# Performance work log

Hardware: AMD Instinct MI355X
Metric: run time of the kernel (lower is better)

## Reference

```python
import jax, jax.numpy as jnp
import numpy as np

RADIUS = 0.1      # ball-query radius; also max_dist in collision_error
THRESH = 0.001    # collision threshold
NSAMPLE = 4       # neighbors per query point
EPS = 1e-7
LOSS_WEIGHT = 1.0


def _face_normals(verts, faces):
    # verts: (b, n_v, 3), faces: (b, n_f, 3) int -> unit face normals (b, n_f, 3)
    tri = jax.vmap(lambda V, F: V[F])(verts, faces)  # (b, n_f, 3verts, 3xyz)
    e1 = tri[:, :, 1] - tri[:, :, 0]
    e2 = tri[:, :, 2] - tri[:, :, 0]
    fn = jnp.cross(e1, e2)
    return fn / (jnp.linalg.norm(fn, axis=-1, keepdims=True) + EPS)


def _vertex_normals(faces, fn, n_v):
    # sparse v2f bmm equivalent: average incident face normals per vertex
    def scatter(F, N):
        idx = F.reshape(-1)                    # (3*n_f,) face->vertex ids
        vals = jnp.repeat(N, 3, axis=0)        # each face normal to its 3 verts
        s = jnp.zeros((n_v, 3), N.dtype).at[idx].add(vals)
        c = jnp.zeros((n_v, 1), N.dtype).at[idx].add(jnp.float32(1.0))
        return s / (c + EPS)
    return jax.vmap(scatter)(faces, fn)        # (b, n_v, 3)


def _ball_query(new_xyz, xyz, radius, nsample):
    # PointNet++ ball query: first `nsample` points of xyz within radius of each
    # new_xyz point; unfilled slots repeat the first hit (0 if no hits).
    d2 = jnp.sum((new_xyz[:, :, None, :] - xyz[:, None, :, :]) ** 2, axis=-1)  # (b, nq, nv)
    within = d2 < radius * radius
    c = jnp.cumsum(within.astype(jnp.int32), axis=-1)
    n_within = c[..., -1]
    first_idx = jnp.argmax(within, axis=-1)    # 0 when no hits (matches CUDA kernel)
    slots = []
    for j in range(nsample):
        idx_j = jnp.argmax(within & (c == j + 1), axis=-1)
        slots.append(jnp.where(n_within > j, idx_j, first_idx))
    return jnp.stack(slots, axis=-1)           # (b, nq, nsample)


def _collision_loss(pred, h_state, h_faces):
    faces = jnp.swapaxes(h_faces, 1, 2)                 # (b, n_f, 3)
    human_verts = jnp.swapaxes(h_state, 1, 2)[..., :3]  # (b, n_v, 3)
    n_v = human_verts.shape[1]

    fn = _face_normals(human_verts, faces)
    vn = _vertex_normals(faces, fn, n_v)                # (b, n_v, 3)

    idx = _ball_query(pred, human_verts, RADIUS, NSAMPLE)      # (b, nq, K)
    gxyz = jax.vmap(lambda V, I: V[I])(human_verts, idx)       # (b, nq, K, 3)
    gn = jax.vmap(lambda V, I: V[I])(vn, idx)                  # (b, nq, K, 3)

    diff = pred[:, :, None, :] - gxyz
    gn = gn / (jnp.linalg.norm(gn, axis=-1, keepdims=True) + EPS)
    dot = jnp.sum(diff * gn, axis=-1)                   # (b, nq, K)
    valid_dot = (dot - THRESH) * (dot >= -RADIUS)       # max_dist = radius
    mask = valid_dot < 0
    per_pt = jnp.sum(valid_dot * mask / (jnp.sum(mask, axis=-1, keepdims=True) + EPS), axis=-1) ** 2
    avg_mask = per_pt > 0
    loss = jnp.sum(per_pt)                              # reduction='sum', weight=None
    loss = loss / (jnp.sum(avg_mask) + EPS)
    return LOSS_WEIGHT * loss


def setup_inputs() -> dict:
    key = jax.random.key(0)
    k1, k2, k3, k4 = jax.random.split(key, 4)
    bs, n_pred, n_v, n_f, C = 2, 8192, 6890, 13776, 6
    pred = jax.random.uniform(k1, (bs, n_pred, 3), dtype=jnp.float32)
    label = jax.random.uniform(k2, (bs, n_pred, 3), dtype=jnp.float32)
    h_state = jax.random.uniform(k3, (bs, C, n_v), dtype=jnp.float32)
    h_faces = jax.random.randint(k4, (bs, 3, n_f), 0, n_v, dtype=jnp.int32)
    return {"pred": pred, "label": label, "h_state": h_state, "h_faces": h_faces}


def reference(pred, label, h_state, h_faces):
    # label is unused by collision_error (kept for signature fidelity)
    return _collision_loss(pred, h_state, h_faces)
```

## Files before the change

### kernel.cpp

```cpp
#include <hip/hip_runtime.h>
#include <cstdint>
#include <climits>

#define EPSF 1e-7f
#define NCELL 1000
#define RPAD 0.10002f


__device__ __forceinline__ int cell_of(float x, float y, float z) {
    int cx = min(max((int)(x * 10.0f), 0), 9);
    int cy = min(max((int)(y * 10.0f), 0), 9);
    int cz = min(max((int)(z * 10.0f), 0), 9);
    return (cx * 10 + cy) * 10 + cz;
}

__global__ void k1_face_count(const float* __restrict__ hs,
                              const int* __restrict__ hf,
                              float* __restrict__ svec,
                              float* __restrict__ scnt,
                              int* __restrict__ counts,
                              int n_v, int n_f, int bs) {
    int t = blockIdx.x * blockDim.x + threadIdx.x;
    if (t < bs * n_f) {
        int b = t / n_f;
        int f = t - b * n_f;
        const int* fb = hf + (size_t)b * 3 * n_f;
        int i0 = fb[f];
        int i1 = fb[n_f + f];
        int i2 = fb[2 * n_f + f];
        const float* xs = hs + (size_t)b * 6 * n_v;
        const float* ys = xs + n_v;
        const float* zs = xs + 2 * n_v;
        float ax = xs[i0], ay = ys[i0], az = zs[i0];
        float bx = xs[i1], by = ys[i1], bz = zs[i1];
        float cx = xs[i2], cy = ys[i2], cz = zs[i2];
        float e1x = bx - ax, e1y = by - ay, e1z = bz - az;
        float e2x = cx - ax, e2y = cy - ay, e2z = cz - az;
        float fx = e1y * e2z - e1z * e2y;
        float fy = e1z * e2x - e1x * e2z;
        float fz = e1x * e2y - e1y * e2x;
        float nrm = sqrtf(fx * fx + fy * fy + fz * fz) + EPSF;
        fx /= nrm; fy /= nrm; fz /= nrm;
        float* sb = svec + (size_t)b * n_v * 3;
        float* cb = scnt + (size_t)b * n_v;
        atomicAdd(&sb[i0 * 3 + 0], fx);
        atomicAdd(&sb[i0 * 3 + 1], fy);
        atomicAdd(&sb[i0 * 3 + 2], fz);
        atomicAdd(&sb[i1 * 3 + 0], fx);
        atomicAdd(&sb[i1 * 3 + 1], fy);
        atomicAdd(&sb[i1 * 3 + 2], fz);
        atomicAdd(&sb[i2 * 3 + 0], fx);
        atomicAdd(&sb[i2 * 3 + 1], fy);
        atomicAdd(&sb[i2 * 3 + 2], fz);
        atomicAdd(&cb[i0], 1.0f);
        atomicAdd(&cb[i1], 1.0f);
        atomicAdd(&cb[i2], 1.0f);
    }
    if (t < bs * n_v) {
        int b = t / n_v;
        int v = t - b * n_v;
        const float* xs = hs + (size_t)b * 6 * n_v;
        float x = xs[v], y = xs[n_v + v], z = xs[2 * n_v + v];
        atomicAdd(&counts[b * NCELL + cell_of(x, y, z)], 1);
    }
}

__global__ void k2_build(const float* __restrict__ hs,
                         const float* __restrict__ svec,
                         const float* __restrict__ scnt,
                         const int* __restrict__ counts,
                         int* __restrict__ cellstart,
                         float4* __restrict__ vert,
                         float4* __restrict__ spk,
                         int n_v, int bs, int nvb) {
    __shared__ int cursor_l[NCELL];
    if (blockIdx.x < (unsigned)nvb) {
        int t = blockIdx.x * blockDim.x + threadIdx.x;
        if (t >= bs * n_v) return;
        int b = t / n_v;
        int v = t - b * n_v;
        float cc = scnt[t] + EPSF;
        float vx = svec[t * 3 + 0] / cc;
        float vy = svec[t * 3 + 1] / cc;
        float vz = svec[t * 3 + 2] / cc;
        float nrm = sqrtf(vx * vx + vy * vy + vz * vz) + EPSF;
        const float* xs = hs + (size_t)b * 6 * n_v;
        float x = xs[v], y = xs[n_v + v], z = xs[2 * n_v + v];
        vert[2 * (size_t)t + 0] = make_float4(x, y, z, 0.0f);
        vert[2 * (size_t)t + 1] = make_float4(vx / nrm, vy / nrm, vz / nrm, 0.0f);
        return;
    }
    int batch = blockIdx.x - nvb;
    if (threadIdx.x < 64) {
        int lane = threadIdx.x;
        int local[16];
        int mysum = 0;
        #pragma unroll
        for (int k = 0; k < 16; ++k) {
            int c = lane * 16 + k;
            int v = (c < NCELL) ? counts[batch * NCELL + c] : 0;
            local[k] = v;
            mysum += v;
        }
        int s = mysum;
        #pragma unroll
        for (int off = 1; off < 64; off <<= 1) {
            int n = __shfl_up(s, off);
            if (lane >= off) s += n;
        }
        int excl = s - mysum;
        #pragma unroll
        for (int k = 0; k < 16; ++k) {
            int c = lane * 16 + k;
            if (c < NCELL) {
                cellstart[batch * (NCELL + 1) + c] = excl;
                cursor_l[c] = excl;
                excl += local[k];
            }
        }
        if (lane == 63) cellstart[batch * (NCELL + 1) + NCELL] = s;
    }
    __syncthreads();
    const float* xs = hs + (size_t)batch * 6 * n_v;
    for (int v = threadIdx.x; v < n_v; v += blockDim.x) {
        float x = xs[v], y = xs[n_v + v], z = xs[2 * n_v + v];
        int cell = cell_of(x, y, z);
        int pos = atomicAdd(&cursor_l[cell], 1);
        spk[(size_t)batch * n_v + pos] = make_float4(x, y, z, __int_as_float(v));
    }
}

__global__ __launch_bounds__(256, 8) void k3_query(
                         const float* __restrict__ pred,
                         const float4* __restrict__ vert,
                         const float4* __restrict__ spk,
                         const int* __restrict__ cellstart,
                         double* __restrict__ partial,
                         float* __restrict__ pcnt,
                         int n_v, int n_pred, int bs) {
    const int lane = threadIdx.x & 63;
    const int wave = threadIdx.x >> 6;
    const int sub = lane & 31;
    const int half = lane >> 5;
    const int qid = blockIdx.x * 8 + wave * 2 + half;
    const int nq = bs * n_pred;

    float per_pt = 0.0f;
    float is_pos = 0.0f;

    if (qid < nq) {
        const int b = qid / n_pred;
        const float4* vb = vert + 2 * (size_t)b * n_v;
        const float4* sp = spk + (size_t)b * n_v;
        const int* csb = cellstart + b * (NCELL + 1);
        const float px = pred[(size_t)qid * 3 + 0];
        const float py = pred[(size_t)qid * 3 + 1];
        const float pz = pred[(size_t)qid * 3 + 2];

        int xlo = max(0, (int)floorf((px - RPAD) * 10.0f));
        int xhi = min(9, (int)floorf((px + RPAD) * 10.0f));
        int ylo = max(0, (int)floorf((py - RPAD) * 10.0f));
        int yhi = min(9, (int)floorf((py + RPAD) * 10.0f));
        int zlo = max(0, (int)floorf((pz - RPAD) * 10.0f));
        int zhi = min(9, (int)floorf((pz + RPAD) * 10.0f));

        int ip = min(sub, 8);
        int cxr = xlo + ip / 3;
        int cyr = ylo + ip % 3;
        bool validr = (cxr <= xhi) && (cyr <= yhi) && (sub < 9);
        int rowbase = (min(cxr, 9) * 10 + min(cyr, 9)) * 10;
        int rsv = csb[rowbase + zlo];
        int rev = csb[rowbase + zhi + 1];
        if (!validr) rev = rsv;

        unsigned PK[9];
        #pragma unroll
        for (int i = 0; i < 9; ++i) {
            unsigned rs = (unsigned)__shfl(rsv, i, 32);
            unsigned re = (unsigned)__shfl(rev, i, 32);
            PK[i] = (re << 16) | rs;
        }

        float4 c0[9];
        #pragma unroll
        for (int i = 0; i < 9; ++i) {
            int p = (int)(PK[i] & 0xffffu) + sub;
            c0[i] = sp[(p < (int)(PK[i] >> 16)) ? p : 0];
        }

        int l0 = INT_MAX, l1 = INT_MAX, l2 = INT_MAX, l3 = INT_MAX;
        #pragma unroll
        for (int i = 0; i < 9; ++i) {
            if ((int)(PK[i] & 0xffffu) + sub < (int)(PK[i] >> 16)) {
                float4 c4 = c0[i];
                float dx = px - c4.x;
                float dy = py - c4.y;
                float dz = pz - c4.z;
                float d2 = dx * dx + dy * dy + dz * dz;
                if (d2 < 0.01f) {
                    int vid = __float_as_int(c4.w);
                    if (vid < l3) {
                        if (vid < l1) {
                            if (vid < l0) { l3 = l2; l2 = l1; l1 = l0; l0 = vid; }
                            else          { l3 = l2; l2 = l1; l1 = vid; }
                        } else {
                            if (vid < l2) { l3 = l2; l2 = vid; }
                            else          { l3 = vid; }
                        }
                    }
                }
            }
        }
        #pragma unroll
        for (int i = 0; i < 9; ++i) {
            int re = (int)(PK[i] >> 16);
            for (int p = (int)(PK[i] & 0xffffu) + 32 + sub; p < re; p += 32) {
                float4 c4 = sp[p];
                float dx = px - c4.x;
                float dy = py - c4.y;
                float dz = pz - c4.z;
                float d2 = dx * dx + dy * dy + dz * dz;
                if (d2 < 0.01f) {
                    int vid = __float_as_int(c4.w);
                    if (vid < l3) {
                        if (vid < l1) {
                            if (vid < l0) { l3 = l2; l2 = l1; l1 = l0; l0 = vid; }
                            else          { l3 = l2; l2 = l1; l1 = vid; }
                        } else {
                            if (vid < l2) { l3 = l2; l2 = vid; }
                            else          { l3 = vid; }
                        }
                    }
                }
            }
        }

        #pragma unroll
        for (int off = 1; off < 32; off <<= 1) {
            int r0 = __shfl_xor(l3, off);
            int r1 = __shfl_xor(l2, off);
            int r2 = __shfl_xor(l1, off);
            int r3 = __shfl_xor(l0, off);
            int m0 = min(l0, r0);
            int m1 = min(l1, r1);
            int m2 = min(l2, r2);
            int m3 = min(l3, r3);
            int t0 = min(m0, m2), t2 = max(m0, m2);
            int t1 = min(m1, m3), t3 = max(m1, m3);
            l0 = min(t0, t1); l1 = max(t0, t1);
            l2 = min(t2, t3); l3 = max(t2, t3);
        }

        int id0 = (l0 == INT_MAX) ? 0 : l0;
        int id1 = (l1 == INT_MAX) ? id0 : l1;
        int id2 = (l2 == INT_MAX) ? id0 : l2;
        int id3 = (l3 == INT_MAX) ? id0 : l3;
        int ids[4] = {id0, id1, id2, id3};

        float vd[4];
        float cm = 0.0f;
        #pragma unroll
        for (int j = 0; j < 4; ++j) {
            int id = ids[j];
            float4 cj = vb[2 * id + 0];
            float4 nj = vb[2 * id + 1];
            float dx = px - cj.x;
            float dy = py - cj.y;
            float dz = pz - cj.z;
            float dot = dx * nj.x + dy * nj.y + dz * nj.z;
            float w = (dot >= -0.1f) ? 1.0f : 0.0f;
            float v = (dot - 0.001f) * w;
            bool msk = v < 0.0f;
            vd[j] = msk ? v : 0.0f;
            cm += msk ? 1.0f : 0.0f;
        }
        float s = ((vd[0] + vd[1]) + vd[2]) + vd[3];
        float a = s / (cm + EPSF);
        per_pt = a * a;
        is_pos = (per_pt > 0.0f) ? 1.0f : 0.0f;
    }

    __shared__ float ls[8];
    __shared__ float lc[8];
    if (sub == 0) {
        int slot = wave * 2 + half;
        ls[slot] = per_pt;
        lc[slot] = is_pos;
    }
    __syncthreads();
    if (threadIdx.x == 0) {
        double ssum = 0.0;
        float csum = 0.0f;
        #pragma unroll
        for (int k = 0; k < 8; ++k) {
            ssum += (double)ls[k];
            csum += lc[k];
        }
        partial[blockIdx.x] = ssum;
        pcnt[blockIdx.x] = csum;
    }
}

__global__ void finalize_kernel(const double* __restrict__ partial,
                                const float* __restrict__ pcnt,
                                int n, float* __restrict__ out) {
    double s = 0.0, c = 0.0;
    for (int i = threadIdx.x; i < n; i += blockDim.x) {
        s += partial[i];
        c += (double)pcnt[i];
    }
    #pragma unroll
    for (int off = 32; off > 0; off >>= 1) {
        s += __shfl_down(s, off);
        c += __shfl_down(c, off);
    }
    __shared__ double ws_s[4];
    __shared__ double ws_c[4];
    int wave = threadIdx.x >> 6;
    int lane = threadIdx.x & 63;
    if (lane == 0) { ws_s[wave] = s; ws_c[wave] = c; }
    __syncthreads();
    if (threadIdx.x == 0) {
        double S = ws_s[0] + ws_s[1] + ws_s[2] + ws_s[3];
        double C = ws_c[0] + ws_c[1] + ws_c[2] + ws_c[3];
        out[0] = (float)(S / (C + 1e-7));
    }
}

extern "C" void kernel_launch(void* const* d_in, const int* in_sizes, int n_in,
                              void* d_out, int out_size, void* d_ws, size_t ws_size,
                              hipStream_t stream) {
    const float* pred    = (const float*)d_in[0];
    const float* h_state = (const float*)d_in[2];
    const int*   h_faces = (const int*)d_in[3];
    float* out = (float*)d_out;

    const int bs = 2;
    const int n_pred = in_sizes[0] / (bs * 3);
    const int n_v    = in_sizes[2] / (bs * 6);
    const int n_f    = in_sizes[3] / (bs * 3);
    const int nq = bs * n_pred;
    const int nblk = (nq + 7) / 8;

    size_t o_svec    = 0;
    size_t o_scnt    = o_svec + (size_t)bs * n_v * 3;
    size_t o_counts  = o_scnt + (size_t)bs * n_v;
    size_t o_zeroend = (o_counts + (size_t)bs * NCELL + 3) & ~(size_t)3;
    size_t o_cs      = o_zeroend;
    size_t o_partial = (o_cs + (size_t)bs * (NCELL + 1) + 1) & ~(size_t)1;
    size_t o_pcnt    = o_partial + 2 * (size_t)nblk;
    size_t o_spk     = (o_pcnt + (size_t)nblk + 3) & ~(size_t)3;
    size_t o_vert    = o_spk + (size_t)bs * n_v * 4;

    float* base = (float*)d_ws;
    float*  svec      = base + o_svec;
    float*  scnt      = base + o_scnt;
    int*    counts    = (int*)(base + o_counts);
    int*    cellstart = (int*)(base + o_cs);
    double* partial   = (double*)(base + o_partial);
    float*  pcnt      = base + o_pcnt;
    float4* spk       = (float4*)(base + o_spk);
    float4* vert      = (float4*)(base + o_vert);

    hipMemsetAsync(d_ws, 0, o_zeroend * sizeof(float), stream);

    int t1 = bs * n_f;
    k1_face_count<<<(t1 + 63) / 64, 64, 0, stream>>>(
        h_state, h_faces, svec, scnt, counts, n_v, n_f, bs);

    int nvb = (bs * n_v + 1023) / 1024;
    k2_build<<<nvb + bs, 1024, 0, stream>>>(
        h_state, svec, scnt, counts, cellstart, vert, spk, n_v, bs, nvb);

    k3_query<<<nblk, 256, 0, stream>>>(
        pred, vert, spk, cellstart, partial, pcnt, n_v, n_pred, bs);

    finalize_kernel<<<1, 256, 0, stream>>>(partial, pcnt, nblk, out);
}
```

Baseline: 105.0 us.

## Fuse build kernels with spin-wait, recompute normals in query, last-block finalize

Merges the face-normal/cell-count kernel and the grid-build kernel into one launch. The scan blocks spin on a global counter until every face block has finished. The vertex-normal packing pass is removed: the query kernel now reads the raw sums and counts and normalizes them per neighbor on the fly. The separate finalize kernel is replaced by atomic accumulation into 64 slots, with the last block reducing them. This cuts launches and intermediate buffers, at the cost of a spin-wait that assumes the face blocks are co-resident or scheduled first, more scattered loads in the query, and a non-deterministic summation order. The query kernel's launch_bounds hint is also dropped.

```diff
diff --git a/kernel.cpp b/kernel.cpp
--- a/kernel.cpp
+++ b/kernel.cpp
@@ -14,83 +14,73 @@
     return (cx * 10 + cy) * 10 + cz;
 }
 
-__global__ void k1_face_count(const float* __restrict__ hs,
-                              const int* __restrict__ hf,
-                              float* __restrict__ svec,
-                              float* __restrict__ scnt,
-                              int* __restrict__ counts,
-                              int n_v, int n_f, int bs) {
-    int t = blockIdx.x * blockDim.x + threadIdx.x;
-    if (t < bs * n_f) {
-        int b = t / n_f;
-        int f = t - b * n_f;
-        const int* fb = hf + (size_t)b * 3 * n_f;
-        int i0 = fb[f];
-        int i1 = fb[n_f + f];
-        int i2 = fb[2 * n_f + f];
-        const float* xs = hs + (size_t)b * 6 * n_v;
-        const float* ys = xs + n_v;
-        const float* zs = xs + 2 * n_v;
-        float ax = xs[i0], ay = ys[i0], az = zs[i0];
-        float bx = xs[i1], by = ys[i1], bz = zs[i1];
-        float cx = xs[i2], cy = ys[i2], cz = zs[i2];
-        float e1x = bx - ax, e1y = by - ay, e1z = bz - az;
-        float e2x = cx - ax, e2y = cy - ay, e2z = cz - az;
-        float fx = e1y * e2z - e1z * e2y;
-        float fy = e1z * e2x - e1x * e2z;
-        float fz = e1x * e2y - e1y * e2x;
-        float nrm = sqrtf(fx * fx + fy * fy + fz * fz) + EPSF;
-        fx /= nrm; fy /= nrm; fz /= nrm;
-        float* sb = svec + (size_t)b * n_v * 3;
-        float* cb = scnt + (size_t)b * n_v;
-        atomicAdd(&sb[i0 * 3 + 0], fx);
-        atomicAdd(&sb[i0 * 3 + 1], fy);
-        atomicAdd(&sb[i0 * 3 + 2], fz);
-        atomicAdd(&sb[i1 * 3 + 0], fx);
-        atomicAdd(&sb[i1 * 3 + 1], fy);
-        atomicAdd(&sb[i1 * 3 + 2], fz);
-        atomicAdd(&sb[i2 * 3 + 0], fx);
-        atomicAdd(&sb[i2 * 3 + 1], fy);
-        atomicAdd(&sb[i2 * 3 + 2], fz);
-        atomicAdd(&cb[i0], 1.0f);
-        atomicAdd(&cb[i1], 1.0f);
-        atomicAdd(&cb[i2], 1.0f);
-    }
-    if (t < bs * n_v) {
-        int b = t / n_v;
-        int v = t - b * n_v;
-        const float* xs = hs + (size_t)b * 6 * n_v;
-        float x = xs[v], y = xs[n_v + v], z = xs[2 * n_v + v];
-        atomicAdd(&counts[b * NCELL + cell_of(x, y, z)], 1);
-    }
-}
-
-__global__ void k2_build(const float* __restrict__ hs,
-                         const float* __restrict__ svec,
-                         const float* __restrict__ scnt,
-                         const int* __restrict__ counts,
-                         int* __restrict__ cellstart,
-                         float4* __restrict__ vert,
-                         float4* __restrict__ spk,
-                         int n_v, int bs, int nvb) {
+__global__ void k12_build(const float* __restrict__ hs,
+                          const int* __restrict__ hf,
+                          float* __restrict__ svec,
+                          float* __restrict__ scnt,
+                          int* __restrict__ counts,
+                          int* __restrict__ ctrl,
+                          int* __restrict__ cellstart,
+                          float4* __restrict__ spk,
+                          int n_v, int n_f, int bs, int nfb) {
     __shared__ int cursor_l[NCELL];
-    if (blockIdx.x < (unsigned)nvb) {
-        int t = blockIdx.x * blockDim.x + threadIdx.x;
-        if (t >= bs * n_v) return;
-        int b = t / n_v;
-        int v = t - b * n_v;
-        float cc = scnt[t] + EPSF;
-        float vx = svec[t * 3 + 0] / cc;
-        float vy = svec[t * 3 + 1] / cc;
-        float vz = svec[t * 3 + 2] / cc;
-        float nrm = sqrtf(vx * vx + vy * vy + vz * vz) + EPSF;
-        const float* xs = hs + (size_t)b * 6 * n_v;
-        float x = xs[v], y = xs[n_v + v], z = xs[2 * n_v + v];
-        vert[2 * (size_t)t + 0] = make_float4(x, y, z, 0.0f);
-        vert[2 * (size_t)t + 1] = make_float4(vx / nrm, vy / nrm, vz / nrm, 0.0f);
+    const int blk = blockIdx.x;
+
+    if (blk < nfb) {
+        int t = blk * blockDim.x + threadIdx.x;
+        if (t < bs * n_f) {
+            int b = t / n_f;
+            int f = t - b * n_f;
+            const int* fb = hf + (size_t)b * 3 * n_f;
+            int i0 = fb[f];
+            int i1 = fb[n_f + f];
+            int i2 = fb[2 * n_f + f];
+            const float* xs = hs + (size_t)b * 6 * n_v;
+            const float* ys = xs + n_v;
+            const float* zs = xs + 2 * n_v;
+            float ax = xs[i0], ay = ys[i0], az = zs[i0];
+            float bx = xs[i1], by = ys[i1], bz = zs[i1];
+            float cx = xs[i2], cy = ys[i2], cz = zs[i2];
+            float e1x = bx - ax, e1y = by - ay, e1z = bz - az;
+            float e2x = cx - ax, e2y = cy - ay, e2z = cz - az;
+            float fx = e1y * e2z - e1z * e2y;
+            float fy = e1z * e2x - e1x * e2z;
+            float fz = e1x * e2y - e1y * e2x;
+            float nrm = sqrtf(fx * fx + fy * fy + fz * fz) + EPSF;
+            fx /= nrm; fy /= nrm; fz /= nrm;
+            float* sb = svec + (size_t)b * n_v * 3;
+            float* cb = scnt + (size_t)b * n_v;
+            atomicAdd(&sb[i0 * 3 + 0], fx);
+            atomicAdd(&sb[i0 * 3 + 1], fy);
+            atomicAdd(&sb[i0 * 3 + 2], fz);
+            atomicAdd(&sb[i1 * 3 + 0], fx);
+            atomicAdd(&sb[i1 * 3 + 1], fy);
+            atomicAdd(&sb[i1 * 3 + 2], fz);
+            atomicAdd(&sb[i2 * 3 + 0], fx);
+            atomicAdd(&sb[i2 * 3 + 1], fy);
+            atomicAdd(&sb[i2 * 3 + 2], fz);
+            atomicAdd(&cb[i0], 1.0f);
+            atomicAdd(&cb[i1], 1.0f);
+            atomicAdd(&cb[i2], 1.0f);
+        }
+        if (t < bs * n_v) {
+            int b = t / n_v;
+            int v = t - b * n_v;
+            const float* xs = hs + (size_t)b * 6 * n_v;
+            float x = xs[v], y = xs[n_v + v], z = xs[2 * n_v + v];
+            atomicAdd(&counts[b * NCELL + cell_of(x, y, z)], 1);
+        }
+        __syncthreads();
+        if (threadIdx.x == 0) atomicAdd(&ctrl[0], 1);
         return;
     }
-    int batch = blockIdx.x - nvb;
+
+    const int batch = blk - nfb;
+    if (threadIdx.x == 0) {
+        while (atomicAdd(&ctrl[0], 0) < nfb) {  }
+    }
+    __syncthreads();
+
     if (threadIdx.x < 64) {
         int lane = threadIdx.x;
         int local[16];
@@ -130,13 +120,16 @@
     }
 }
 
-__global__ __launch_bounds__(256, 8) void k3_query(
-                         const float* __restrict__ pred,
-                         const float4* __restrict__ vert,
+__global__ void k3_query(const float* __restrict__ pred,
+                         const float* __restrict__ hs,
+                         const float* __restrict__ svec,
+                         const float* __restrict__ scnt,
                          const float4* __restrict__ spk,
                          const int* __restrict__ cellstart,
-                         double* __restrict__ partial,
-                         float* __restrict__ pcnt,
+                         double* __restrict__ gsum,
+                         float* __restrict__ gcnt,
+                         int* __restrict__ ctrl,
+                         float* __restrict__ out,
                          int n_v, int n_pred, int bs) {
     const int lane = threadIdx.x & 63;
     const int wave = threadIdx.x >> 6;
@@ -150,7 +143,6 @@
 
     if (qid < nq) {
         const int b = qid / n_pred;
-        const float4* vb = vert + 2 * (size_t)b * n_v;
         const float4* sp = spk + (size_t)b * n_v;
         const int* csb = cellstart + b * (NCELL + 1);
         const float px = pred[(size_t)qid * 3 + 0];
@@ -257,17 +249,27 @@
         int id3 = (l3 == INT_MAX) ? id0 : l3;
         int ids[4] = {id0, id1, id2, id3};
 
+        const float* xs = hs + (size_t)b * 6 * n_v;
+        const float* ysv = xs + n_v;
+        const float* zsv = xs + 2 * n_v;
+        const float* svb = svec + (size_t)b * n_v * 3;
+        const float* scb = scnt + (size_t)b * n_v;
+
         float vd[4];
         float cm = 0.0f;
         #pragma unroll
         for (int j = 0; j < 4; ++j) {
             int id = ids[j];
-            float4 cj = vb[2 * id + 0];
-            float4 nj = vb[2 * id + 1];
-            float dx = px - cj.x;
-            float dy = py - cj.y;
-            float dz = pz - cj.z;
-            float dot = dx * nj.x + dy * nj.y + dz * nj.z;
+            float cc = scb[id] + EPSF;
+            float vx = svb[id * 3 + 0] / cc;
+            float vy = svb[id * 3 + 1] / cc;
+            float vz = svb[id * 3 + 2] / cc;
+            float nrm = sqrtf(vx * vx + vy * vy + vz * vz) + EPSF;
+            float njx = vx / nrm, njy = vy / nrm, njz = vz / nrm;
+            float dx = px - xs[id];
+            float dy = py - ysv[id];
+            float dz = pz - zsv[id];
+            float dot = dx * njx + dy * njy + dz * njz;
             float w = (dot >= -0.1f) ? 1.0f : 0.0f;
             float v = (dot - 0.001f) * w;
             bool msk = v < 0.0f;
@@ -282,6 +284,7 @@
 
     __shared__ float ls[8];
     __shared__ float lc[8];
+    __shared__ int lastflag;
     if (sub == 0) {
         int slot = wave * 2 + half;
         ls[slot] = per_pt;
@@ -296,34 +299,25 @@
             ssum += (double)ls[k];
             csum += lc[k];
         }
-        partial[blockIdx.x] = ssum;
-        pcnt[blockIdx.x] = csum;
-    }
-}
-
-__global__ void finalize_kernel(const double* __restrict__ partial,
-                                const float* __restrict__ pcnt,
-                                int n, float* __restrict__ out) {
-    double s = 0.0, c = 0.0;
-    for (int i = threadIdx.x; i < n; i += blockDim.x) {
-        s += partial[i];
-        c += (double)pcnt[i];
-    }
-    #pragma unroll
-    for (int off = 32; off > 0; off >>= 1) {
-        s += __shfl_down(s, off);
-        c += __shfl_down(c, off);
-    }
-    __shared__ double ws_s[4];
-    __shared__ double ws_c[4];
-    int wave = threadIdx.x >> 6;
-    int lane = threadIdx.x & 63;
-    if (lane == 0) { ws_s[wave] = s; ws_c[wave] = c; }
+        double o1 = atomicAdd(&gsum[blockIdx.x & 63], ssum);
+        float  o2 = atomicAdd(&gcnt[blockIdx.x & 63], csum);
+        float oo = (float)o1 + o2;
+        asm volatile("" : : "v"(oo) : "memory");
+        int old = atomicAdd(&ctrl[1], 1);
+        lastflag = (old == (int)gridDim.x - 1) ? 1 : 0;
+    }
     __syncthreads();
-    if (threadIdx.x == 0) {
-        double S = ws_s[0] + ws_s[1] + ws_s[2] + ws_s[3];
-        double C = ws_c[0] + ws_c[1] + ws_c[2] + ws_c[3];
-        out[0] = (float)(S / (C + 1e-7));
+    if (lastflag) {
+        if (threadIdx.x < 64) {
+            double s = atomicAdd(&gsum[threadIdx.x], 0.0);
+            double c = (double)atomicAdd(&gcnt[threadIdx.x], 0.0f);
+            #pragma unroll
+            for (int off = 32; off > 0; off >>= 1) {
+                s += __shfl_down(s, off);
+                c += __shfl_down(c, off);
+            }
+            if (threadIdx.x == 0) out[0] = (float)(s / (c + 1e-7));
+        }
     }
 }
 
@@ -341,39 +335,35 @@
     const int n_f    = in_sizes[3] / (bs * 3);
     const int nq = bs * n_pred;
     const int nblk = (nq + 7) / 8;
+    const int nfb  = (bs * n_f + 511) / 512;
 
     size_t o_svec    = 0;
     size_t o_scnt    = o_svec + (size_t)bs * n_v * 3;
     size_t o_counts  = o_scnt + (size_t)bs * n_v;
-    size_t o_zeroend = (o_counts + (size_t)bs * NCELL + 3) & ~(size_t)3;
+    size_t o_ctrl    = o_counts + (size_t)bs * NCELL;
+    size_t o_gsum    = (o_ctrl + 2 + 1) & ~(size_t)1;
+    size_t o_gcnt    = o_gsum + 2 * 64;
+    size_t o_zeroend = (o_gcnt + 64 + 3) & ~(size_t)3;
     size_t o_cs      = o_zeroend;
-    size_t o_partial = (o_cs + (size_t)bs * (NCELL + 1) + 1) & ~(size_t)1;
-    size_t o_pcnt    = o_partial + 2 * (size_t)nblk;
-    size_t o_spk     = (o_pcnt + (size_t)nblk + 3) & ~(size_t)3;
-    size_t o_vert    = o_spk + (size_t)bs * n_v * 4;
+    size_t o_spk     = (o_cs + (size_t)bs * (NCELL + 1) + 3) & ~(size_t)3;
 
     float* base = (float*)d_ws;
     float*  svec      = base + o_svec;
     float*  scnt      = base + o_scnt;
     int*    counts    = (int*)(base + o_counts);
+    int*    ctrl      = (int*)(base + o_ctrl);
+    double* gsum      = (double*)(base + o_gsum);
+    float*  gcnt      = base + o_gcnt;
     int*    cellstart = (int*)(base + o_cs);
-    double* partial   = (double*)(base + o_partial);
-    float*  pcnt      = base + o_pcnt;
     float4* spk       = (float4*)(base + o_spk);
-    float4* vert      = (float4*)(base + o_vert);
 
     hipMemsetAsync(d_ws, 0, o_zeroend * sizeof(float), stream);
 
-    int t1 = bs * n_f;
-    k1_face_count<<<(t1 + 63) / 64, 64, 0, stream>>>(
-        h_state, h_faces, svec, scnt, counts, n_v, n_f, bs);
-
-    int nvb = (bs * n_v + 1023) / 1024;
-    k2_build<<<nvb + bs, 1024, 0, stream>>>(
-        h_state, svec, scnt, counts, cellstart, vert, spk, n_v, bs, nvb);
+    k12_build<<<nfb + bs, 512, 0, stream>>>(
+        h_state, h_faces, svec, scnt, counts, ctrl, cellstart, spk,
+        n_v, n_f, bs, nfb);
 
     k3_query<<<nblk, 256, 0, stream>>>(
-        pred, vert, spk, cellstart, partial, pcnt, n_v, n_pred, bs);
-
-    finalize_kernel<<<1, 256, 0, stream>>>(partial, pcnt, nblk, out);
+        pred, h_state, svec, scnt, spk, cellstart, gsum, gcnt, ctrl, out,
+        n_v, n_pred, bs);
 }
```

Result: slower. 122.6 us (+16.8%).
